# Kernel tuning notes

Hardware: AMD Instinct MI355X
Metric: run time of the kernel (lower is better)

The kernel has to match this reference:

```python
import jax, jax.numpy as jnp
import numpy as np

T, B, D, A, L = 256, 256, 512, 32, 3
EPS = 1e-6

def _layernorm(x, scale, bias):
    mu = jnp.mean(x, axis=-1, keepdims=True)
    var = jnp.mean(jnp.square(x - mu), axis=-1, keepdims=True)
    return (x - mu) * jax.lax.rsqrt(var + EPS) * scale + bias

def setup_inputs() -> dict:
    key = jax.random.key(0)
    ks = jax.random.split(key, 16)
    def orth(k, shape, scale):
        a = jax.random.normal(k, shape, dtype=jnp.float32)
        q, r = jnp.linalg.qr(a)
        q = q * jnp.sign(jnp.diagonal(r))
        return (scale * q).astype(jnp.float32)
    inp = {
        'hidden': jnp.zeros((B, D), jnp.float32),
        'obs': jax.random.normal(ks[0], (T, B, D), jnp.float32),
        'dones': jax.random.randint(ks[1], (T, B), 0, 2) > 0,
        'avail_actions': jax.random.randint(ks[2], (T, B, A), 0, 2).astype(jnp.int32),
        # MLP stack: 3 Dense(D) + LayerNorm
        'Wm': jnp.stack([orth(jax.random.fold_in(ks[3], l), (D, D), np.sqrt(2)) for l in range(L)]),
        'bm': jnp.zeros((L, D), jnp.float32),
        'lns': jnp.ones((L, D), jnp.float32),
        'lnb': jnp.zeros((L, D), jnp.float32),
        # GRUCell params: input denses ir/iz/in (with bias), hidden denses hr/hz (no bias), hn (bias)
        'Wi': jnp.stack([jax.random.normal(jax.random.fold_in(ks[4], g), (D, D), jnp.float32) / np.sqrt(D) for g in range(3)]),
        'bi': jnp.zeros((3, D), jnp.float32),
        'Wh': jnp.stack([orth(jax.random.fold_in(ks[5], g), (D, D), 1.0) for g in range(3)]),
        'bhn': jnp.zeros((D,), jnp.float32),
        # actor head
        'Wo': orth(ks[6], (D, D), 2.0),
        'bo': jnp.zeros((D,), jnp.float32),
        'ln2s': jnp.ones((D,), jnp.float32),
        'ln2b': jnp.zeros((D,), jnp.float32),
        'Wa': orth(ks[7], (D, A), 0.01),
        'ba': jnp.zeros((A,), jnp.float32),
    }
    return inp

def reference(hidden, obs, dones, avail_actions, Wm, bm, lns, lnb, Wi, bi, Wh, bhn, Wo, bo, ln2s, ln2b, Wa, ba):
    # MLP encoder: Dense -> LayerNorm -> ReLU, x num_layers
    e = obs  # [T,B,D]
    for l in range(Wm.shape[0]):
        e = jax.nn.relu(_layernorm(e @ Wm[l] + bm[l], lns[l], lnb[l]))
    # time-scanned GRU with reset-masked carry (reset -> zeros carry)
    def step(h, xs):
        x, d = xs  # x:[B,D], d:[B]
        h = jnp.where(d[:, None], jnp.zeros_like(h), h)
        r = jax.nn.sigmoid(x @ Wi[0] + bi[0] + h @ Wh[0])
        z = jax.nn.sigmoid(x @ Wi[1] + bi[1] + h @ Wh[1])
        n = jnp.tanh(x @ Wi[2] + bi[2] + r * (h @ Wh[2] + bhn))
        h_new = (1.0 - z) * n + z * h
        return h_new, h_new
    hidden, y = jax.lax.scan(step, hidden, (e, dones))  # y:[T,B,D]
    # actor head
    am = jax.nn.relu(_layernorm(y @ Wo + bo, ln2s, ln2b))
    logits = am @ Wa + ba
    unavail = 1.0 - avail_actions.astype(logits.dtype)
    action_logits = logits - unavail * 1e10
    return hidden, action_logits
```

## Files before the change

### kernel.cpp

```cpp
#include <hip/hip_runtime.h>
#include <hip/hip_bf16.h>
#include <math.h>


#define TTT 256
#define BBB 256
#define DDD 512
#define ACT 32
#define MMM (TTT*BBB)

typedef short bf16x8 __attribute__((ext_vector_type(8)));
typedef float f32x4 __attribute__((ext_vector_type(4)));
typedef unsigned short u16;

__device__ inline u16 f2bf(float f) {
    unsigned int u = __float_as_uint(f);
    u += 0x7fffu + ((u >> 16) & 1u);
    return (u16)(u >> 16);
}
__device__ inline float bf2f(u16 h) { return __uint_as_float(((unsigned int)h) << 16); }

__global__ __launch_bounds__(256) void transpose_cvt_k(
    const float* __restrict__ in, u16* __restrict__ out, int ostride)
{
    __shared__ float tile[32][33];
    const int c = threadIdx.x & 31;
    const int r0 = threadIdx.x >> 5;
    const int bx = blockIdx.x, by = blockIdx.y;
#pragma unroll
    for (int p = 0; p < 4; p++) {
        int r = r0 + p * 8;
        tile[r][c] = in[(size_t)(by * 32 + r) * DDD + bx * 32 + c];
    }
    __syncthreads();
#pragma unroll
    for (int p = 0; p < 4; p++) {
        int r = r0 + p * 8;
        out[(size_t)(bx * 32 + r) * ostride + by * 32 + c] = f2bf(tile[c][r]);
    }
}

template<bool AF32>
__global__ __launch_bounds__(256) void gemm_bf16_k(
    const void* __restrict__ Aptr, const u16* __restrict__ Bt,
    const float* __restrict__ bias, u16* __restrict__ C, int N)
{
    __shared__ u16 As[128 * 64];
    __shared__ u16 Bs[128 * 64];
    const int tid = threadIdx.x;
    const int row0 = blockIdx.x * 128;
    const int col0 = blockIdx.y * 128;
    const int lane = tid & 63, wid = tid >> 6;
    const int wr = wid >> 1, wc = wid & 1;
    const int lm = lane & 15, lq = lane >> 4;

    f32x4 acc[4][4];
#pragma unroll
    for (int i = 0; i < 4; i++)
#pragma unroll
        for (int j = 0; j < 4; j++) acc[i][j] = (f32x4){0.f, 0.f, 0.f, 0.f};

    for (int kc = 0; kc < 8; kc++) {
        const int k0 = kc * 64;
#pragma unroll
        for (int p = 0; p < 4; p++) {
            int g = p * 256 + tid;
            int row = g >> 3, j = g & 7;
            bf16x8 v;
            if (AF32) {
                const float* s = (const float*)Aptr + (size_t)(row0 + row) * DDD + k0 + j * 8;
                float4 a0 = *(const float4*)s;
                float4 a1 = *(const float4*)(s + 4);
                v[0] = (short)f2bf(a0.x); v[1] = (short)f2bf(a0.y);
                v[2] = (short)f2bf(a0.z); v[3] = (short)f2bf(a0.w);
                v[4] = (short)f2bf(a1.x); v[5] = (short)f2bf(a1.y);
                v[6] = (short)f2bf(a1.z); v[7] = (short)f2bf(a1.w);
            } else {
                v = *(const bf16x8*)((const u16*)Aptr + (size_t)(row0 + row) * DDD + k0 + j * 8);
            }
            *(bf16x8*)(As + row * 64 + ((j ^ (row & 7)) << 3)) = v;
        }
#pragma unroll
        for (int p = 0; p < 4; p++) {
            int g = p * 256 + tid;
            int n = g >> 3, j = g & 7;
            bf16x8 v = *(const bf16x8*)(Bt + (size_t)(col0 + n) * DDD + k0 + j * 8);
            *(bf16x8*)(Bs + n * 64 + ((j ^ (n & 7)) << 3)) = v;
        }
        __syncthreads();
#pragma unroll
        for (int ks = 0; ks < 2; ks++) {
            bf16x8 af[4], bfr[4];
#pragma unroll
            for (int i = 0; i < 4; i++) {
                int row = wr * 64 + i * 16 + lm;
                af[i] = *(const bf16x8*)(As + row * 64 + (((ks * 4 + lq) ^ (row & 7)) << 3));
            }
#pragma unroll
            for (int j = 0; j < 4; j++) {
                int n = wc * 64 + j * 16 + lm;
                bfr[j] = *(const bf16x8*)(Bs + n * 64 + (((ks * 4 + lq) ^ (n & 7)) << 3));
            }
#pragma unroll
            for (int i = 0; i < 4; i++)
#pragma unroll
                for (int j = 0; j < 4; j++)
                    acc[i][j] = __builtin_amdgcn_mfma_f32_16x16x32_bf16(af[i], bfr[j], acc[i][j], 0, 0, 0);
        }
        __syncthreads();
    }
#pragma unroll
    for (int j = 0; j < 4; j++) {
        int col = col0 + wc * 64 + j * 16 + lm;
        float bj = bias[col];
#pragma unroll
        for (int i = 0; i < 4; i++) {
            int rb = row0 + wr * 64 + i * 16 + lq * 4;
#pragma unroll
            for (int r = 0; r < 4; r++)
                C[(size_t)(rb + r) * N + col] = f2bf(acc[i][j][r] + bj);
        }
    }
}

__global__ __launch_bounds__(256) void ln_relu_k(
    u16* __restrict__ X, const float* __restrict__ gamma, const float* __restrict__ beta)
{
    const int tid = threadIdx.x;
    const int lane = tid & 63;
    const size_t row = (size_t)blockIdx.x * 4 + (tid >> 6);
    const int c0 = lane * 8;
    u16* px = X + row * DDD + c0;
    bf16x8 v = *(const bf16x8*)px;
    float f[8]; float s = 0.f, s2 = 0.f;
#pragma unroll
    for (int i = 0; i < 8; i++) { f[i] = bf2f((u16)v[i]); s += f[i]; s2 += f[i] * f[i]; }
#pragma unroll
    for (int off = 32; off; off >>= 1) { s += __shfl_xor(s, off); s2 += __shfl_xor(s2, off); }
    float mu = s * (1.f / (float)DDD);
    float rs = rsqrtf(s2 * (1.f / (float)DDD) - mu * mu + 1e-6f);
    float4 g0 = *(const float4*)(gamma + c0), g1 = *(const float4*)(gamma + c0 + 4);
    float4 b0 = *(const float4*)(beta + c0),  b1 = *(const float4*)(beta + c0 + 4);
    float gg[8] = {g0.x, g0.y, g0.z, g0.w, g1.x, g1.y, g1.z, g1.w};
    float bb[8] = {b0.x, b0.y, b0.z, b0.w, b1.x, b1.y, b1.z, b1.w};
    bf16x8 o;
#pragma unroll
    for (int i = 0; i < 8; i++) {
        float yv = (f[i] - mu) * rs * gg[i] + bb[i];
        o[i] = (short)f2bf(fmaxf(yv, 0.f));
    }
    *(bf16x8*)px = o;
}

__global__ __launch_bounds__(256) void logits_k(
    const u16* __restrict__ AM, const float* __restrict__ Wa,
    const float* __restrict__ ba, const int* __restrict__ avail,
    float* __restrict__ out)
{
    __shared__ float xs[8][DDD];
    const int tid = threadIdx.x;
    const size_t row0 = (size_t)blockIdx.x * 8;
    for (int g = tid; g < 8 * 64; g += 256) {
        int r = g >> 6, c8 = (g & 63) * 8;
        bf16x8 v = *(const bf16x8*)(AM + (row0 + r) * DDD + c8);
#pragma unroll
        for (int i = 0; i < 8; i++) xs[r][c8 + i] = bf2f((u16)v[i]);
    }
    __syncthreads();
    const int r = tid >> 5, a = tid & 31;
    float acc = 0.f;
    for (int k = 0; k < DDD; k += 4) {
        float4 xv = *(const float4*)&xs[r][k];
        acc = fmaf(xv.x, Wa[(k + 0) * ACT + a], acc);
        acc = fmaf(xv.y, Wa[(k + 1) * ACT + a], acc);
        acc = fmaf(xv.z, Wa[(k + 2) * ACT + a], acc);
        acc = fmaf(xv.w, Wa[(k + 3) * ACT + a], acc);
    }
    size_t o = (row0 + r) * ACT + a;
    float v = acc + ba[a];
    if (avail[o] == 0) v -= 1e10f;
    out[o] = v;
}

__global__ __launch_bounds__(256) void depth_build_k(
    const int* __restrict__ dones,
    int* __restrict__ depthA, int* __restrict__ pidxA,
    int* __restrict__ counts, int* __restrict__ maxd)
{
    __shared__ int lc[256];
    __shared__ int lmax;
    const int b = threadIdx.x;
    lc[b] = 0;
    if (b == 0) lmax = 0;
    __syncthreads();
    int dprev = 0, mx = 0;
    for (int t = 0; t < TTT; t++) {
        int pos = t * BBB + b;
        int d, pi;
        if (dones[pos] != 0)       { d = 0; pi = -1; }
        else if (t == 0)           { d = 0; pi = -2 - b; }
        else                       { d = dprev + 1; pi = pos - BBB; }
        depthA[pos] = d; pidxA[pos] = pi;
        atomicAdd(&lc[d], 1);
        mx = max(mx, d);
        dprev = d;
    }
    atomicMax(&lmax, mx);
    __syncthreads();
    counts[b] = lc[b];
    if (b == 0) *maxd = lmax;
}

__global__ void scan_k(const int* __restrict__ counts, int* __restrict__ offs)
{
    if (threadIdx.x == 0) {
        int s = 0;
        for (int i = 0; i < 256; i++) { offs[i] = s; s += counts[i]; }
    }
}

__global__ __launch_bounds__(256) void scatter_k(
    const int* __restrict__ depthA, const int* __restrict__ offs,
    int* __restrict__ cursor, int* __restrict__ list)
{
    __shared__ int lcnt[256];
    __shared__ int lbase[256];
    const int tid = threadIdx.x;
    lcnt[tid] = 0;
    __syncthreads();
    int pos = blockIdx.x * 256 + tid;
    int d = depthA[pos];
    int rank = atomicAdd(&lcnt[d], 1);
    __syncthreads();
    int c = lcnt[tid];
    lbase[tid] = c ? atomicAdd(&cursor[tid], c) : 0;
    __syncthreads();
    list[offs[d] + lbase[d] + rank] = pos;
}

__device__ inline void grid_barrier(int* cnt, int* gen, int nblk)
{
    __syncthreads();
    if (threadIdx.x == 0) {
        __threadfence();
        int g = __hip_atomic_load(gen, __ATOMIC_RELAXED, __HIP_MEMORY_SCOPE_AGENT);
        int a = __hip_atomic_fetch_add(cnt, 1, __ATOMIC_ACQ_REL, __HIP_MEMORY_SCOPE_AGENT);
        if (a == nblk - 1) {
            __hip_atomic_store(cnt, 0, __ATOMIC_RELAXED, __HIP_MEMORY_SCOPE_AGENT);
            __hip_atomic_store(gen, g + 1, __ATOMIC_RELEASE, __HIP_MEMORY_SCOPE_AGENT);
        } else {
            while (__hip_atomic_load(gen, __ATOMIC_RELAXED, __HIP_MEMORY_SCOPE_AGENT) == g)
                __builtin_amdgcn_s_sleep(4);
            (void)__hip_atomic_load(gen, __ATOMIC_ACQUIRE, __HIP_MEMORY_SCOPE_AGENT);
        }
        __threadfence();
    }
    __syncthreads();
}

template<bool YF32>
__global__ __launch_bounds__(256, 2) void gru_depth_k(
    const u16* __restrict__ E, const float* __restrict__ hidden,
    const u16* __restrict__ Wstk, const float* __restrict__ bi,
    const float* __restrict__ bhn,
    const int* __restrict__ list, const int* __restrict__ offs,
    const int* __restrict__ counts, const int* __restrict__ maxd,
    const int* __restrict__ pidxA,
    void* __restrict__ Yv, float* __restrict__ hid_out,
    int* __restrict__ barCnt, int* __restrict__ barGen)
{
    __shared__ u16 As[64 * 256];
    __shared__ int posL[64], pidxL[64];
    __shared__ int sAnyH;
    const int tid = threadIdx.x;
    const int w = tid >> 6, lane = tid & 63;
    const int lm = lane & 15, lq = lane >> 4;
    const int nblk = gridDim.x;

    const int MD = *maxd;
    for (int d = 0; d <= MD; d++) {
        const int nd = counts[d];
        const int off = offs[d];
        const int njobs = ((nd + 63) >> 6) << 2;
        for (int j = blockIdx.x; j < njobs; j += nblk) {
            const int rt = j >> 2, panel = j & 3;
            bool hasH = false;
            if (tid < 64) {
                int idx = rt * 64 + tid;
                int p = (idx < nd) ? list[off + idx] : -1;
                int pi = (p >= 0) ? pidxA[p] : -1;
                posL[tid] = p;
                pidxL[tid] = pi;
                hasH = (p >= 0) && (pi != -1);
            }
            if (tid < 64) {
                unsigned long long m = __ballot(hasH);
                if (tid == 0) sAnyH = (m != 0ULL);
            }
            __syncthreads();
            const bool skipH = !sAnyH;

            f32x4 a01[4][4], aX[4][2], aH[4][2];
#pragma unroll
            for (int mt = 0; mt < 4; mt++) {
#pragma unroll
                for (int q = 0; q < 4; q++) a01[mt][q] = (f32x4){0.f, 0.f, 0.f, 0.f};
#pragma unroll
                for (int q = 0; q < 2; q++) {
                    aX[mt][q] = (f32x4){0.f, 0.f, 0.f, 0.f};
                    aH[mt][q] = (f32x4){0.f, 0.f, 0.f, 0.f};
                }
            }

            const int cb = panel * 128 + w * 32;
            const u16* wp[6];
#pragma unroll
            for (int ct = 0; ct < 6; ct++) {
                int gate = ct >> 1;
                int nglob = gate * 512 + cb + ((ct & 1) << 4) + lm;
                wp[ct] = Wstk + (size_t)nglob * 1024 + lq * 8;
            }

            const int nkc = skipH ? 2 : 4;
            for (int kc = 0; kc < nkc; kc++) {
#pragma unroll
                for (int it = 0; it < 8; it++) {
                    int g = it * 256 + tid;
                    int row = g >> 5, jg = g & 31;
                    int kglob = kc * 256 + jg * 8;
                    bf16x8 v = (bf16x8){0, 0, 0, 0, 0, 0, 0, 0};
                    int p = posL[row];
                    if (p >= 0) {
                        if (kglob < 512) {
                            v = *(const bf16x8*)(E + (size_t)p * DDD + kglob);
                        } else {
                            int k2 = kglob - 512;
                            int pi = pidxL[row];
                            if (pi >= 0) {
                                if (YF32) {
                                    const float* s = (const float*)Yv + (size_t)pi * DDD + k2;
                                    float4 a0 = *(const float4*)s;
                                    float4 a1 = *(const float4*)(s + 4);
                                    v[0] = (short)f2bf(a0.x); v[1] = (short)f2bf(a0.y);
                                    v[2] = (short)f2bf(a0.z); v[3] = (short)f2bf(a0.w);
                                    v[4] = (short)f2bf(a1.x); v[5] = (short)f2bf(a1.y);
                                    v[6] = (short)f2bf(a1.z); v[7] = (short)f2bf(a1.w);
                                } else {
                                    v = *(const bf16x8*)((const u16*)Yv + (size_t)pi * DDD + k2);
                                }
                            } else if (pi <= -2) {
                                const float* s = hidden + (size_t)(-pi - 2) * DDD + k2;
                                float4 a0 = *(const float4*)s;
                                float4 a1 = *(const float4*)(s + 4);
                                v[0] = (short)f2bf(a0.x); v[1] = (short)f2bf(a0.y);
                                v[2] = (short)f2bf(a0.z); v[3] = (short)f2bf(a0.w);
                                v[4] = (short)f2bf(a1.x); v[5] = (short)f2bf(a1.y);
                                v[6] = (short)f2bf(a1.z); v[7] = (short)f2bf(a1.w);
                            }
                        }
                    }
                    *(bf16x8*)(As + row * 256 + ((jg ^ (row & 31)) << 3)) = v;
                }
                __syncthreads();

                const bool xpart = (kc < 2);
                const int kgb = kc * 256;
                bf16x8 bfA[6], bfB[6];

#define LOADW(B, KG) \
    _Pragma("unroll") \
    for (int ct = 0; ct < 6; ct++) B[ct] = *(const bf16x8*)(wp[ct] + (KG));

#define COMPW(B, S) \
    _Pragma("unroll") \
    for (int mt = 0; mt < 4; mt++) { \
        int row = mt * 16 + lm; \
        int jgr = (S) * 4 + lq; \
        bf16x8 af = *(const bf16x8*)(As + row * 256 + ((jgr ^ (row & 31)) << 3)); \
        a01[mt][0] = __builtin_amdgcn_mfma_f32_16x16x32_bf16(af, B[0], a01[mt][0], 0, 0, 0); \
        a01[mt][1] = __builtin_amdgcn_mfma_f32_16x16x32_bf16(af, B[1], a01[mt][1], 0, 0, 0); \
        a01[mt][2] = __builtin_amdgcn_mfma_f32_16x16x32_bf16(af, B[2], a01[mt][2], 0, 0, 0); \
        a01[mt][3] = __builtin_amdgcn_mfma_f32_16x16x32_bf16(af, B[3], a01[mt][3], 0, 0, 0); \
        if (xpart) { \
            aX[mt][0] = __builtin_amdgcn_mfma_f32_16x16x32_bf16(af, B[4], aX[mt][0], 0, 0, 0); \
            aX[mt][1] = __builtin_amdgcn_mfma_f32_16x16x32_bf16(af, B[5], aX[mt][1], 0, 0, 0); \
        } else { \
            aH[mt][0] = __builtin_amdgcn_mfma_f32_16x16x32_bf16(af, B[4], aH[mt][0], 0, 0, 0); \
            aH[mt][1] = __builtin_amdgcn_mfma_f32_16x16x32_bf16(af, B[5], aH[mt][1], 0, 0, 0); \
        } \
    }

                LOADW(bfA, kgb + 0 * 32);
#pragma unroll
                for (int sp = 0; sp < 4; sp++) {
                    const int s0 = sp * 2, s1 = sp * 2 + 1;
                    LOADW(bfB, kgb + s1 * 32);
                    COMPW(bfA, s0);
                    if (sp < 3) { LOADW(bfA, kgb + (s1 + 1) * 32); }
                    COMPW(bfB, s1);
                }
#undef LOADW
#undef COMPW
                __syncthreads();
            }

#pragma unroll
            for (int mt = 0; mt < 4; mt++) {
#pragma unroll
                for (int r = 0; r < 4; r++) {
                    int row = mt * 16 + lq * 4 + r;
                    int p = posL[row];
                    if (p < 0) continue;
                    int pi = pidxL[row];
#pragma unroll
                    for (int ct = 0; ct < 2; ct++) {
                        int cglob = cb + ct * 16 + lm;
                        float rpre = a01[mt][ct][r]     + bi[cglob];
                        float zpre = a01[mt][2 + ct][r] + bi[512 + cglob];
                        float xn   = aX[mt][ct][r]      + bi[1024 + cglob];
                        float hn   = aH[mt][ct][r]      + bhn[cglob];
                        float rg = 1.f / (1.f + __expf(-rpre));
                        float zg = 1.f / (1.f + __expf(-zpre));
                        float targ = xn + rg * hn;
                        float t2 = __expf(-2.f * fabsf(targ));
                        float ng = copysignf((1.f - t2) / (1.f + t2), targ);
                        float hp = 0.f;
                        if (pi >= 0)
                            hp = YF32 ? ((const float*)Yv)[(size_t)pi * DDD + cglob]
                                      : bf2f(((const u16*)Yv)[(size_t)pi * DDD + cglob]);
                        else if (pi <= -2)
                            hp = hidden[(size_t)(-pi - 2) * DDD + cglob];
                        float hnew = (1.f - zg) * ng + zg * hp;
                        if (YF32) ((float*)Yv)[(size_t)p * DDD + cglob] = hnew;
                        else      ((u16*)Yv)[(size_t)p * DDD + cglob] = f2bf(hnew);
                    }
                }
            }
            __syncthreads();
        }
        grid_barrier(barCnt, barGen, nblk);
    }

    for (int i = blockIdx.x * 256 + tid; i < BBB * DDD; i += nblk * 256) {
        int b = i >> 9, c = i & 511;
        size_t yi = (size_t)(65280 + b) * DDD + c;
        hid_out[i] = YF32 ? ((const float*)Yv)[yi] : bf2f(((const u16*)Yv)[yi]);
    }
}

extern "C" void kernel_launch(void* const* d_in, const int* in_sizes, int n_in,
                              void* d_out, int out_size, void* d_ws, size_t ws_size,
                              hipStream_t stream)
{
    const float* hidden = (const float*)d_in[0];
    const float* obs    = (const float*)d_in[1];
    const int*   dones  = (const int*)d_in[2];
    const int*   avail  = (const int*)d_in[3];
    const float* Wm     = (const float*)d_in[4];
    const float* bm     = (const float*)d_in[5];
    const float* lns    = (const float*)d_in[6];
    const float* lnb    = (const float*)d_in[7];
    const float* Wi     = (const float*)d_in[8];
    const float* bi     = (const float*)d_in[9];
    const float* Wh     = (const float*)d_in[10];
    const float* bhn    = (const float*)d_in[11];
    const float* Wo     = (const float*)d_in[12];
    const float* bo     = (const float*)d_in[13];
    const float* ln2s   = (const float*)d_in[14];
    const float* ln2b   = (const float*)d_in[15];
    const float* Wa     = (const float*)d_in[16];
    const float* ba     = (const float*)d_in[17];
    float* out = (float*)d_out;

    char* w = (char*)d_ws;
    u16* Wstk = (u16*)w;  w += (size_t)1536 * 1024 * 2;
    u16* WmT  = (u16*)w;  w += (size_t)3 * DDD * DDD * 2;
    u16* WoT  = (u16*)w;  w += (size_t)DDD * DDD * 2;
    int* meta = (int*)w;  w += 4096;
    int* counts = meta, *offs = meta + 256, *cursor = meta + 512, *maxd = meta + 768;
    int* barCnt = meta + 800, *barGen = meta + 832;
    int* depthA = (int*)w;  w += (size_t)MMM * 4;
    int* pidxA  = (int*)w;  w += (size_t)MMM * 4;
    int* list   = (int*)w;  w += (size_t)MMM * 4;
    u16* P = (u16*)w;       w += (size_t)MMM * DDD * 2;
    void* Yv = (void*)w;
    const size_t base = (size_t)(w - (char*)d_ws);
    const bool yf32 = (ws_size >= base + (size_t)MMM * DDD * 4);

    dim3 tgrid(16, 16);
    for (int l = 0; l < 3; l++)
        transpose_cvt_k<<<tgrid, 256, 0, stream>>>(Wm + (size_t)l * DDD * DDD, WmT + (size_t)l * DDD * DDD, DDD);
    transpose_cvt_k<<<tgrid, 256, 0, stream>>>(Wo, WoT, DDD);
    for (int g = 0; g < 3; g++) {
        transpose_cvt_k<<<tgrid, 256, 0, stream>>>(Wi + (size_t)g * DDD * DDD, Wstk + (size_t)g * 512 * 1024, 1024);
        transpose_cvt_k<<<tgrid, 256, 0, stream>>>(Wh + (size_t)g * DDD * DDD, Wstk + (size_t)g * 512 * 1024 + 512, 1024);
    }
    hipMemsetAsync(meta, 0, 4096, stream);

    depth_build_k<<<1, 256, 0, stream>>>(dones, depthA, pidxA, counts, maxd);
    scan_k<<<1, 64, 0, stream>>>(counts, offs);
    scatter_k<<<MMM / 256, 256, 0, stream>>>(depthA, offs, cursor, list);

    u16* Yq = (u16*)Yv;
    gemm_bf16_k<true><<<dim3(MMM / 128, 4), 256, 0, stream>>>(obs, WmT, bm, P, DDD);
    ln_relu_k<<<dim3(MMM / 4), 256, 0, stream>>>(P, lns, lnb);
    gemm_bf16_k<false><<<dim3(MMM / 128, 4), 256, 0, stream>>>(P, WmT + (size_t)DDD * DDD, bm + DDD, Yq, DDD);
    ln_relu_k<<<dim3(MMM / 4), 256, 0, stream>>>(Yq, lns + DDD, lnb + DDD);
    gemm_bf16_k<false><<<dim3(MMM / 128, 4), 256, 0, stream>>>(Yq, WmT + (size_t)2 * DDD * DDD, bm + 2 * DDD, P, DDD);
    ln_relu_k<<<dim3(MMM / 4), 256, 0, stream>>>(P, lns + 2 * DDD, lnb + 2 * DDD);

    {
        const void* fptr = yf32 ? (const void*)gru_depth_k<true>
                                : (const void*)gru_depth_k<false>;
        int occ = 0;
        hipError_t e = hipOccupancyMaxActiveBlocksPerMultiprocessor(&occ, fptr, 256, 0);
        if (e != hipSuccess || occ < 1) occ = 2;
        if (occ > 4) occ = 4;
        dim3 grid(occ * 256);
        if (yf32)
            gru_depth_k<true><<<grid, 256, 0, stream>>>(
                P, hidden, Wstk, bi, bhn, list, offs, counts, maxd, pidxA,
                Yv, out, barCnt, barGen);
        else
            gru_depth_k<false><<<grid, 256, 0, stream>>>(
                P, hidden, Wstk, bi, bhn, list, offs, counts, maxd, pidxA,
                Yv, out, barCnt, barGen);
    }

    if (yf32)
        gemm_bf16_k<true><<<dim3(MMM / 128, 4), 256, 0, stream>>>(Yv, WoT, bo, P, DDD);
    else
        gemm_bf16_k<false><<<dim3(MMM / 128, 4), 256, 0, stream>>>(Yv, WoT, bo, P, DDD);
    ln_relu_k<<<dim3(MMM / 4), 256, 0, stream>>>(P, ln2s, ln2b);
    logits_k<<<dim3(MMM / 8), 256, 0, stream>>>(P, Wa, ba, avail, out + BBB * DDD);
}
```

Before: 2.163 ms.

## Split depth-0 rows into reset and initial-hidden buckets; map tiles to XCD-local blocks

The depth key now separates rows reset by dones (zero carry) from t=0 rows that start from the given hidden state. Reset rows land in their own bucket, so whole tiles of them can skip the hidden-state GEMM. The GRU job loop also assigns each row tile to a fixed group of blocks (blockIdx & 7), so all four panels of a tile, and tiles with the same residue, run on the same XCD and should reuse its L2. This adds one more grid-barrier level and doubles the metadata arrays, and it can unbalance work when there are few tiles.

```diff
diff --git a/kernel.cpp b/kernel.cpp
--- a/kernel.cpp
+++ b/kernel.cpp
@@ -184,58 +184,61 @@
 
 __global__ __launch_bounds__(256) void depth_build_k(
     const int* __restrict__ dones,
-    int* __restrict__ depthA, int* __restrict__ pidxA,
-    int* __restrict__ counts, int* __restrict__ maxd)
-{
-    __shared__ int lc[256];
+    int* __restrict__ keyA, int* __restrict__ pidxA,
+    int* __restrict__ counts, int* __restrict__ maxk)
+{
+    __shared__ int lc[512];
     __shared__ int lmax;
     const int b = threadIdx.x;
-    lc[b] = 0;
+    lc[b] = 0; lc[b + 256] = 0;
     if (b == 0) lmax = 0;
     __syncthreads();
     int dprev = 0, mx = 0;
     for (int t = 0; t < TTT; t++) {
         int pos = t * BBB + b;
-        int d, pi;
-        if (dones[pos] != 0)       { d = 0; pi = -1; }
-        else if (t == 0)           { d = 0; pi = -2 - b; }
-        else                       { d = dprev + 1; pi = pos - BBB; }
-        depthA[pos] = d; pidxA[pos] = pi;
-        atomicAdd(&lc[d], 1);
-        mx = max(mx, d);
+        int d, pi, k;
+        if (dones[pos] != 0)       { d = 0; pi = -1;       k = 0; }
+        else if (t == 0)           { d = 0; pi = -2 - b;   k = 1; }
+        else                       { d = dprev + 1; pi = pos - BBB; k = d + 1; }
+        keyA[pos] = k; pidxA[pos] = pi;
+        atomicAdd(&lc[k], 1);
+        mx = max(mx, k);
         dprev = d;
     }
     atomicMax(&lmax, mx);
     __syncthreads();
     counts[b] = lc[b];
-    if (b == 0) *maxd = lmax;
+    counts[b + 256] = lc[b + 256];
+    if (b == 0) *maxk = lmax;
 }
 
 __global__ void scan_k(const int* __restrict__ counts, int* __restrict__ offs)
 {
     if (threadIdx.x == 0) {
         int s = 0;
-        for (int i = 0; i < 256; i++) { offs[i] = s; s += counts[i]; }
+        for (int i = 0; i < 512; i++) { offs[i] = s; s += counts[i]; }
     }
 }
 
 __global__ __launch_bounds__(256) void scatter_k(
-    const int* __restrict__ depthA, const int* __restrict__ offs,
+    const int* __restrict__ keyA, const int* __restrict__ offs,
     int* __restrict__ cursor, int* __restrict__ list)
 {
-    __shared__ int lcnt[256];
-    __shared__ int lbase[256];
+    __shared__ int lcnt[512];
+    __shared__ int lbase[512];
     const int tid = threadIdx.x;
-    lcnt[tid] = 0;
+    lcnt[tid] = 0; lcnt[tid + 256] = 0;
     __syncthreads();
     int pos = blockIdx.x * 256 + tid;
-    int d = depthA[pos];
-    int rank = atomicAdd(&lcnt[d], 1);
-    __syncthreads();
-    int c = lcnt[tid];
-    lbase[tid] = c ? atomicAdd(&cursor[tid], c) : 0;
-    __syncthreads();
-    list[offs[d] + lbase[d] + rank] = pos;
+    int k = keyA[pos];
+    int rank = atomicAdd(&lcnt[k], 1);
+    __syncthreads();
+    for (int q = tid; q < 512; q += 256) {
+        int c = lcnt[q];
+        lbase[q] = c ? atomicAdd(&cursor[q], c) : 0;
+    }
+    __syncthreads();
+    list[offs[k] + lbase[k] + rank] = pos;
 }
 
 __device__ inline void grid_barrier(int* cnt, int* gen, int nblk)
@@ -264,7 +267,7 @@
     const u16* __restrict__ Wstk, const float* __restrict__ bi,
     const float* __restrict__ bhn,
     const int* __restrict__ list, const int* __restrict__ offs,
-    const int* __restrict__ counts, const int* __restrict__ maxd,
+    const int* __restrict__ counts, const int* __restrict__ maxk,
     const int* __restrict__ pidxA,
     void* __restrict__ Yv, float* __restrict__ hid_out,
     int* __restrict__ barCnt, int* __restrict__ barGen)
@@ -276,14 +279,20 @@
     const int w = tid >> 6, lane = tid & 63;
     const int lm = lane & 15, lq = lane >> 4;
     const int nblk = gridDim.x;
-
-    const int MD = *maxd;
-    for (int d = 0; d <= MD; d++) {
-        const int nd = counts[d];
-        const int off = offs[d];
-        const int njobs = ((nd + 63) >> 6) << 2;
-        for (int j = blockIdx.x; j < njobs; j += nblk) {
-            const int rt = j >> 2, panel = j & 3;
+    const int e   = blockIdx.x & 7;
+    const int xb  = blockIdx.x >> 3;
+    const int nxb = nblk >> 3;
+
+    const int MK = *maxk;
+    for (int k = 0; k <= MK; k++) {
+        const int nd = counts[k];
+        const int off = offs[k];
+        const int ntiles = (nd + 63) >> 6;
+        const int ntl = (ntiles - e + 7) >> 3;
+        const int njl = (ntl > 0) ? (ntl << 2) : 0;
+        for (int lj = xb; lj < njl; lj += nxb) {
+            const int rt = ((lj >> 2) << 3) + e;
+            const int panel = lj & 3;
             bool hasH = false;
             if (tid < 64) {
                 int idx = rt * 64 + tid;
@@ -292,8 +301,6 @@
                 posL[tid] = p;
                 pidxL[tid] = pi;
                 hasH = (p >= 0) && (pi != -1);
-            }
-            if (tid < 64) {
                 unsigned long long m = __ballot(hasH);
                 if (tid == 0) sAnyH = (m != 0ULL);
             }
@@ -476,10 +483,14 @@
     u16* Wstk = (u16*)w;  w += (size_t)1536 * 1024 * 2;
     u16* WmT  = (u16*)w;  w += (size_t)3 * DDD * DDD * 2;
     u16* WoT  = (u16*)w;  w += (size_t)DDD * DDD * 2;
-    int* meta = (int*)w;  w += 4096;
-    int* counts = meta, *offs = meta + 256, *cursor = meta + 512, *maxd = meta + 768;
-    int* barCnt = meta + 800, *barGen = meta + 832;
-    int* depthA = (int*)w;  w += (size_t)MMM * 4;
+    int* meta = (int*)w;  w += 8192;
+    int* counts = meta;
+    int* offs   = meta + 512;
+    int* cursor = meta + 1024;
+    int* maxk   = meta + 1536;
+    int* barCnt = meta + 1568;
+    int* barGen = meta + 1600;
+    int* keyA   = (int*)w;  w += (size_t)MMM * 4;
     int* pidxA  = (int*)w;  w += (size_t)MMM * 4;
     int* list   = (int*)w;  w += (size_t)MMM * 4;
     u16* P = (u16*)w;       w += (size_t)MMM * DDD * 2;
@@ -495,11 +506,11 @@
         transpose_cvt_k<<<tgrid, 256, 0, stream>>>(Wi + (size_t)g * DDD * DDD, Wstk + (size_t)g * 512 * 1024, 1024);
         transpose_cvt_k<<<tgrid, 256, 0, stream>>>(Wh + (size_t)g * DDD * DDD, Wstk + (size_t)g * 512 * 1024 + 512, 1024);
     }
-    hipMemsetAsync(meta, 0, 4096, stream);
-
-    depth_build_k<<<1, 256, 0, stream>>>(dones, depthA, pidxA, counts, maxd);
+    hipMemsetAsync(meta, 0, 8192, stream);
+
+    depth_build_k<<<1, 256, 0, stream>>>(dones, keyA, pidxA, counts, maxk);
     scan_k<<<1, 64, 0, stream>>>(counts, offs);
-    scatter_k<<<MMM / 256, 256, 0, stream>>>(depthA, offs, cursor, list);
+    scatter_k<<<MMM / 256, 256, 0, stream>>>(keyA, offs, cursor, list);
 
     u16* Yq = (u16*)Yv;
     gemm_bf16_k<true><<<dim3(MMM / 128, 4), 256, 0, stream>>>(obs, WmT, bm, P, DDD);
@@ -519,11 +530,11 @@
         dim3 grid(occ * 256);
         if (yf32)
             gru_depth_k<true><<<grid, 256, 0, stream>>>(
-                P, hidden, Wstk, bi, bhn, list, offs, counts, maxd, pidxA,
+                P, hidden, Wstk, bi, bhn, list, offs, counts, maxk, pidxA,
                 Yv, out, barCnt, barGen);
         else
             gru_depth_k<false><<<grid, 256, 0, stream>>>(
-                P, hidden, Wstk, bi, bhn, list, offs, counts, maxd, pidxA,
+                P, hidden, Wstk, bi, bhn, list, offs, counts, maxk, pidxA,
                 Yv, out, barCnt, barGen);
     }
 
```

Measured after the change: 2.181 ms. About the same (+0.8%).
